# Kernel tuning notes

Hardware: AMD Instinct MI355X
Metric: run time of the kernel (lower is better)

The kernel has to match this reference:

```python
import jax, jax.numpy as jnp
import numpy as np

EPS = 1e-5


def setup_inputs() -> dict:
    key = jax.random.key(0)
    ks = jax.random.split(key, 6)
    b, n, x_len, h_len = 128, 512, 512, 512
    fan_in = x_len + h_len
    std = float(np.sqrt(2.0 / fan_in))  # kaiming_normal_ for [h_len, x_len+h_len]
    X = jax.random.normal(ks[0], (b, n, x_len), dtype=jnp.float32)
    W_a = jax.random.normal(ks[1], (h_len, fan_in), dtype=jnp.float32) * std
    W_g = jax.random.normal(ks[2], (h_len, fan_in), dtype=jnp.float32) * std
    b_a = jax.random.normal(ks[3], (h_len,), dtype=jnp.float32) * 0.02
    b_g = jax.random.normal(ks[4], (h_len,), dtype=jnp.float32) * 0.02
    gamma = jnp.ones((h_len,), dtype=jnp.float32)
    beta = jnp.zeros((h_len,), dtype=jnp.float32)
    return {"X": X, "W_a": W_a, "W_g": W_g, "b_a": b_a, "b_g": b_g,
            "gamma": gamma, "beta": beta}


def _layernorm(x, gamma, beta):
    mu = jnp.mean(x, axis=-1, keepdims=True)
    var = jnp.mean(jnp.square(x - mu), axis=-1, keepdims=True)
    return (x - mu) * jax.lax.rsqrt(var + EPS) * gamma + beta


def reference(X, W_a, W_g, b_a, b_g, gamma, beta):
    # X: [b, n, x_len]; recurrent scan over the time axis n.
    b, n, x_len = X.shape
    h_len = W_a.shape[0]

    def step(h, x_t):
        cat = jnp.concatenate([h, x_t], axis=-1)          # [b, h+x]
        alpha = jax.nn.sigmoid(cat @ W_g.T + b_g)          # [b, h]
        a = cat @ W_a.T + b_a                              # [b, h]
        h_tilde = alpha * jnp.tanh(a) + (1.0 - alpha) * a  # affine blend
        h_new = _layernorm(h_tilde, gamma, beta)           # dropout = identity (eval)
        return h_new, h_new

    h0 = jnp.zeros((b, h_len), dtype=X.dtype)
    _, ys = jax.lax.scan(step, h0, jnp.swapaxes(X, 0, 1))  # ys: [n, b, h]
    return jnp.swapaxes(ys, 0, 1)                          # [b, n, h]
```

## Files before the change

### kernel.cpp

```cpp
#include <hip/hip_runtime.h>
#include <math.h>

typedef _Float16 f16;
typedef _Float16 f16x8 __attribute__((ext_vector_type(8)));
typedef float f32x4 __attribute__((ext_vector_type(4)));
typedef unsigned long long u64;
typedef unsigned u32;

union U32H2 { unsigned u; f16 h[2]; };
union UV4H8 { uint4 u; f16x8 h; f16 e[8]; };

#define LN_EPS 1e-5f

__device__ __forceinline__ void st_u64g(u64* p, u64 v) {
    __hip_atomic_store(p, v, __ATOMIC_RELAXED, __HIP_MEMORY_SCOPE_AGENT);
}
__device__ __forceinline__ u64 ld_u64g(const u64* p) {
    return __hip_atomic_load(p, __ATOMIC_RELAXED, __HIP_MEMORY_SCOPE_AGENT);
}

__global__ __launch_bounds__(256) void init_ex(u64* p, int n) {
    const int i = blockIdx.x * 256 + threadIdx.x;
    if (i < n) p[i] = 0ull;
}

__global__ __launch_bounds__(256) void pack_wfrags(
    const float* __restrict__ Wa, const float* __restrict__ Wg,
    const float* __restrict__ gamma, uint4* __restrict__ WP)
{
    const int t = blockIdx.x * 256 + threadIdx.x;
    const int lane = t & 63;
    const int kf = (t >> 6) & 15;
    const int tile = t >> 10;
    const float* W = (tile < 32) ? Wa : Wg;
    const int col = (tile & 31) * 16 + (lane & 15);
    const int k0 = kf * 32 + (lane >> 4) * 8;
    const float* src = W + (size_t)col * 1024 + k0;
    UV4H8 u;
#pragma unroll
    for (int j = 0; j < 8; ++j) u.e[j] = (f16)(src[j] * gamma[k0 + j]);
    WP[t] = u.u;
}

__global__ __launch_bounds__(256) void pack_wx(
    const float* __restrict__ Wa, const float* __restrict__ Wg,
    uint4* __restrict__ WPx)
{
    const int t = blockIdx.x * 256 + threadIdx.x;
    const int lane = t & 63;
    const int kf = (t >> 6) & 15;
    const int tile = t >> 10;
    const float* W = (tile < 32) ? Wa : Wg;
    const int col = (tile & 31) * 16 + (lane & 15);
    const int k0 = kf * 32 + (lane >> 4) * 8;
    const float* src = W + (size_t)col * 1024 + 512 + k0;
    UV4H8 u;
#pragma unroll
    for (int j = 0; j < 8; ++j) u.e[j] = (f16)src[j];
    WPx[t] = u.u;
}

__global__ __launch_bounds__(64) void precompute_consts(
    const float* __restrict__ Wa, const float* __restrict__ Wg,
    const float* __restrict__ gamma, const float* __restrict__ beta,
    float* __restrict__ Cvec)
{
    const int o = blockIdx.x;
    const int l = threadIdx.x;
    const float* wa = Wa + (size_t)o * 1024;
    const float* wg = Wg + (size_t)o * 1024;
    float ca = 0.f, ga = 0.f, cg = 0.f, gg = 0.f;
    for (int k = l; k < 512; k += 64) {
        const float bk = beta[k], gk = gamma[k], a = wa[k], g = wg[k];
        ca += a * bk; ga += a * gk; cg += g * bk; gg += g * gk;
    }
#pragma unroll
    for (int m = 1; m < 64; m <<= 1) {
        ca += __shfl_xor(ca, m); ga += __shfl_xor(ga, m);
        cg += __shfl_xor(cg, m); gg += __shfl_xor(gg, m);
    }
    if (l == 0) {
        Cvec[o] = ca; Cvec[512 + o] = ga; Cvec[1024 + o] = cg; Cvec[1536 + o] = gg;
    }
}

__global__ __launch_bounds__(512) void pgemm16(
    const float* __restrict__ X, const uint4* __restrict__ WPx,
    const float* __restrict__ ba, const float* __restrict__ bg,
    float* __restrict__ Pa, f16* __restrict__ Pgh)
{
    __shared__ f16 As[128 * 64];
    const int tid = threadIdx.x;
    const int wv = tid >> 6, lane = tid & 63;
    const int bid = blockIdx.x;
    const int bn = bid & 7;
    const int bm = bid >> 3;
    const int m0 = bm * 128;
    const int tile = bn * 8 + wv;

    f16x8 Bf[16];
#pragma unroll
    for (int kf = 0; kf < 16; ++kf) {
        UV4H8 uu; uu.u = WPx[(size_t)(tile * 16 + kf) * 64 + lane];
        Bf[kf] = uu.h;
    }
    const int tcol = lane & 15;
    const float bias = (tile < 32) ? ba[tile * 16 + tcol]
                                   : bg[(tile - 32) * 16 + tcol];

    f32x4 acc[8];
#pragma unroll
    for (int mt = 0; mt < 8; ++mt) acc[mt] = (f32x4){0.f, 0.f, 0.f, 0.f};

    const int r = tid >> 2;
    const int c16 = (tid & 3) * 16;
    const int swzw = (r & 7) << 4;
    char* wbase = (char*)As + r * 128;
    const int arow = lane & 15;
    const int swzr = (arow & 7) << 4;
    const int hi = (lane >> 4) * 16;

    for (int kc = 0; kc < 8; ++kc) {
        {
            const float* src = X + (size_t)(m0 + r) * 512 + kc * 64 + c16;
            const float4 v0 = *(const float4*)(src);
            const float4 v1 = *(const float4*)(src + 4);
            const float4 v2 = *(const float4*)(src + 8);
            const float4 v3 = *(const float4*)(src + 12);
            UV4H8 o0, o1;
            o0.e[0] = (f16)v0.x; o0.e[1] = (f16)v0.y; o0.e[2] = (f16)v0.z; o0.e[3] = (f16)v0.w;
            o0.e[4] = (f16)v1.x; o0.e[5] = (f16)v1.y; o0.e[6] = (f16)v1.z; o0.e[7] = (f16)v1.w;
            o1.e[0] = (f16)v2.x; o1.e[1] = (f16)v2.y; o1.e[2] = (f16)v2.z; o1.e[3] = (f16)v2.w;
            o1.e[4] = (f16)v3.x; o1.e[5] = (f16)v3.y; o1.e[6] = (f16)v3.z; o1.e[7] = (f16)v3.w;
            *(uint4*)(wbase + ((c16 * 2) ^ swzw)) = o0.u;
            *(uint4*)(wbase + ((c16 * 2 + 16) ^ swzw)) = o1.u;
        }
        __syncthreads();
#pragma unroll
        for (int mt = 0; mt < 8; ++mt) {
            const char* rbase = (const char*)As + (mt * 16 + arow) * 128;
            const f16x8 Af0 = *(const f16x8*)(rbase + ((hi) ^ swzr));
            acc[mt] = __builtin_amdgcn_mfma_f32_16x16x32_f16(Af0, Bf[kc * 2], acc[mt], 0, 0, 0);
            const f16x8 Af1 = *(const f16x8*)(rbase + ((64 + hi) ^ swzr));
            acc[mt] = __builtin_amdgcn_mfma_f32_16x16x32_f16(Af1, Bf[kc * 2 + 1], acc[mt], 0, 0, 0);
        }
        __syncthreads();
    }

    const int drow = (lane >> 4) * 4;
    if (tile < 32) {
        const int col = tile * 16 + tcol;
#pragma unroll
        for (int mt = 0; mt < 8; ++mt)
#pragma unroll
            for (int i = 0; i < 4; ++i)
                Pa[(size_t)(m0 + mt * 16 + drow + i) * 512 + col] = acc[mt][i] + bias;
    } else {
        const int col = (tile - 32) * 16 + tcol;
#pragma unroll
        for (int mt = 0; mt < 8; ++mt)
#pragma unroll
            for (int i = 0; i < 4; ++i)
                Pgh[(size_t)(m0 + mt * 16 + drow + i) * 512 + col] = (f16)(acc[mt][i] + bias);
    }
}

__global__ __launch_bounds__(512, 1) void scan11(
    const uint4* __restrict__ WP, const float* __restrict__ gamma,
    const float* __restrict__ beta, const float* __restrict__ Cvec,
    float* po, const f16* __restrict__ Pgh,
    u64* __restrict__ THex)
{
    __shared__ f16 hn[16][512];
    __shared__ float Dx[16][132];

    const int tid = threadIdx.x;
    const int wv = tid >> 6, lane = tid & 63;
    const int bid = blockIdx.x;
    const int rg = bid >> 3, cb = bid & 7;
    const int c0 = cb * 64, r0 = rg * 16;

    const int tile = (wv < 4) ? (cb * 4 + wv) : (32 + cb * 4 + (wv - 4));
    f16x8 Bf[16];
#pragma unroll
    for (int kf = 0; kf < 16; ++kf) {
        UV4H8 uu; uu.u = WP[(size_t)(tile * 16 + kf) * 64 + lane];
        Bf[kf] = uu.h;
    }

    for (int i = tid; i < 16 * 256; i += 512) ((unsigned*)hn)[i] = 0u;

    const int rb = tid >> 5, u = tid & 31;
    const int col0 = c0 + 2 * u;
    const float Ca0 = Cvec[col0],        Ca1 = Cvec[col0 + 1];
    const float Ga0 = Cvec[512 + col0],  Ga1 = Cvec[512 + col0 + 1];
    const float Cg0 = Cvec[1024 + col0], Cg1 = Cvec[1024 + col0 + 1];
    const float Gg0 = Cvec[1536 + col0], Gg1 = Cvec[1536 + col0 + 1];
    const float gm0 = gamma[col0], gm1 = gamma[col0 + 1];
    const float bt0 = beta[col0],  bt1 = beta[col0 + 1];

    const int arow = lane & 15;
    const int hi16 = (lane >> 4) * 16;
    const int swzr = (arow & 7) << 4;
    const int swzw = (rb & 7) << 4;
    const char* hrow_r = (const char*)&hn[arow][0];
    char* hrow_w = (char*)&hn[rb][0];
    const int dr = (lane >> 4) * 4;
    const int dc = wv * 16 + (lane & 15);
    const size_t row = (size_t)(r0 + rb);

    u64* pub0 = THex + ((size_t)0 * 8 + rg) * 4096 + (size_t)rb * 256 + cb * 32 + u;
    u64* pub1 = THex + ((size_t)1 * 8 + rg) * 4096 + (size_t)rb * 256 + cb * 32 + u;
    const u64* pol0 = THex + ((size_t)0 * 8 + rg) * 4096 + (size_t)rb * 256 + u;
    const u64* pol1 = THex + ((size_t)1 * 8 + rg) * 4096 + (size_t)rb * 256 + u;

    float ht0, ht1;
    {
        const size_t orow = (row * 512 + 0) * 512 + col0;
        const float2 pa = *(const float2*)(po + orow);
        U32H2 pg; pg.u = *(const unsigned*)(Pgh + orow);
        const float a0 = pa.x, a1 = pa.y;
        const float g0 = (float)pg.h[0], g1 = (float)pg.h[1];
        const float al0 = 1.f / (1.f + __expf(-g0));
        const float al1 = 1.f / (1.f + __expf(-g1));
        const float ac0 = fminf(fmaxf(a0, -15.f), 15.f);
        const float ac1 = fminf(fmaxf(a1, -15.f), 15.f);
        const float e0 = __expf(2.f * ac0), e1 = __expf(2.f * ac1);
        const float th0 = (e0 - 1.f) / (e0 + 1.f);
        const float th1 = (e1 - 1.f) / (e1 + 1.f);
        ht0 = al0 * (th0 - a0) + a0;
        ht1 = al1 * (th1 - a1) + a1;
        U32H2 hw; hw.h[0] = (f16)ht0; hw.h[1] = (f16)ht1;
        st_u64g(pub0, ((u64)1u << 32) | (u64)hw.u);
    }

    for (int t = 1; t < 512; ++t) {
        const unsigned tg = (unsigned)t;
        const u64* hp = ((t - 1) & 1) ? pol1 : pol0;
        const size_t orow = (row * 512 + (size_t)t) * 512 + col0;
        const float2 pa = *(const float2*)(po + orow);
        U32H2 pg; pg.u = *(const unsigned*)(Pgh + orow);

        u64 v[8];
        for (;;) {
#pragma unroll
            for (int i = 0; i < 8; ++i) v[i] = ld_u64g(hp + i * 32);
            bool ok = true;
#pragma unroll
            for (int i = 0; i < 8; ++i) ok &= ((unsigned)(v[i] >> 32) == tg);
            if (ok) break;
        }

        float s1 = 0.f, s2 = 0.f;
#pragma unroll
        for (int i = 0; i < 8; ++i) {
            U32H2 hh; hh.u = (unsigned)v[i];
            const float x0 = (float)hh.h[0], x1 = (float)hh.h[1];
            s1 += x0 + x1; s2 += x0 * x0 + x1 * x1;
            *(u32*)(hrow_w + ((128 * i + 4 * u) ^ swzw)) = (unsigned)v[i];
        }
        __syncthreads();

#pragma unroll
        for (int m = 1; m < 32; m <<= 1) { s1 += __shfl_xor(s1, m); s2 += __shfl_xor(s2, m); }
        const float mu = s1 * (1.f / 512.f);
        const float var = s2 * (1.f / 512.f) - mu * mu;
        const float rs = rsqrtf(fmaxf(var, 0.f) + LN_EPS);
        const float murs = mu * rs;

        f32x4 acc0 = {0.f, 0.f, 0.f, 0.f};
        f32x4 acc1 = {0.f, 0.f, 0.f, 0.f};
#pragma unroll
        for (int kf = 0; kf < 8; ++kf) {
            const f16x8 Af0 = *(const f16x8*)(hrow_r + ((kf * 64 + hi16) ^ swzr));
            acc0 = __builtin_amdgcn_mfma_f32_16x16x32_f16(Af0, Bf[kf], acc0, 0, 0, 0);
            const f16x8 Af1 = *(const f16x8*)(hrow_r + (((kf + 8) * 64 + hi16) ^ swzr));
            acc1 = __builtin_amdgcn_mfma_f32_16x16x32_f16(Af1, Bf[kf + 8], acc1, 0, 0, 0);
        }
        Dx[dr + 0][dc] = acc0[0] + acc1[0];
        Dx[dr + 1][dc] = acc0[1] + acc1[1];
        Dx[dr + 2][dc] = acc0[2] + acc1[2];
        Dx[dr + 3][dc] = acc0[3] + acc1[3];
        __syncthreads();

        const float a0 = rs * Dx[rb][2 * u]          - murs * Ga0 + Ca0 + pa.x;
        const float a1 = rs * Dx[rb][2 * u + 1]      - murs * Ga1 + Ca1 + pa.y;
        const float g0 = rs * Dx[rb][64 + 2 * u]     - murs * Gg0 + Cg0 + (float)pg.h[0];
        const float g1 = rs * Dx[rb][64 + 2 * u + 1] - murs * Gg1 + Cg1 + (float)pg.h[1];
        const float al0 = 1.f / (1.f + __expf(-g0));
        const float al1 = 1.f / (1.f + __expf(-g1));
        const float ac0 = fminf(fmaxf(a0, -15.f), 15.f);
        const float ac1 = fminf(fmaxf(a1, -15.f), 15.f);
        const float e0 = __expf(2.f * ac0), e1 = __expf(2.f * ac1);
        const float th0 = (e0 - 1.f) / (e0 + 1.f);
        const float th1 = (e1 - 1.f) / (e1 + 1.f);
        const float nt0 = al0 * (th0 - a0) + a0;
        const float nt1 = al1 * (th1 - a1) + a1;

        {
            U32H2 hw; hw.h[0] = (f16)nt0; hw.h[1] = (f16)nt1;
            st_u64g((t & 1) ? pub1 : pub0,
                    ((u64)(unsigned)(t + 1) << 32) | (u64)hw.u);
            po[orow - 512]     = (ht0 - mu) * rs * gm0 + bt0;
            po[orow - 512 + 1] = (ht1 - mu) * rs * gm1 + bt1;
            ht0 = nt0; ht1 = nt1;
        }
        __syncthreads();
    }

    {
        u64 v[8];
        for (;;) {
#pragma unroll
            for (int i = 0; i < 8; ++i) v[i] = ld_u64g(pol1 + i * 32);
            bool ok = true;
#pragma unroll
            for (int i = 0; i < 8; ++i) ok &= ((unsigned)(v[i] >> 32) == 512u);
            if (ok) break;
        }
        float s1 = 0.f, s2 = 0.f;
#pragma unroll
        for (int i = 0; i < 8; ++i) {
            U32H2 hh; hh.u = (unsigned)v[i];
            const float x0 = (float)hh.h[0], x1 = (float)hh.h[1];
            s1 += x0 + x1; s2 += x0 * x0 + x1 * x1;
        }
#pragma unroll
        for (int m = 1; m < 32; m <<= 1) { s1 += __shfl_xor(s1, m); s2 += __shfl_xor(s2, m); }
        const float mu = s1 * (1.f / 512.f);
        const float var = s2 * (1.f / 512.f) - mu * mu;
        const float rs = rsqrtf(fmaxf(var, 0.f) + LN_EPS);
        const size_t orow = (row * 512 + 511) * 512 + col0;
        po[orow]     = (ht0 - mu) * rs * gm0 + bt0;
        po[orow + 1] = (ht1 - mu) * rs * gm1 + bt1;
    }
}

extern "C" void kernel_launch(void* const* d_in, const int* in_sizes, int n_in,
                              void* d_out, int out_size, void* d_ws, size_t ws_size,
                              hipStream_t stream) {
    (void)in_sizes; (void)n_in; (void)out_size; (void)ws_size;
    const float* X     = (const float*)d_in[0];
    const float* Wa    = (const float*)d_in[1];
    const float* Wg    = (const float*)d_in[2];
    const float* ba    = (const float*)d_in[3];
    const float* bg    = (const float*)d_in[4];
    const float* gamma = (const float*)d_in[5];
    const float* beta  = (const float*)d_in[6];
    float* out = (float*)d_out;

    char* ws = (char*)d_ws;
    f16*    Pgh  = (f16*)ws;
    uint4*  WP   = (uint4*)(ws + 67108864);
    u64*    THex = (u64*)(ws + 68157440);
    float*  Cvec = (float*)(ws + 68681728);
    uint4*  WPx  = (uint4*)(ws + 68689920);

    init_ex<<<dim3(256), dim3(256), 0, stream>>>(THex, 65536);
    pack_wfrags<<<dim3(256), dim3(256), 0, stream>>>(Wa, Wg, gamma, WP);
    pack_wx<<<dim3(256), dim3(256), 0, stream>>>(Wa, Wg, WPx);
    precompute_consts<<<dim3(512), dim3(64), 0, stream>>>(Wa, Wg, gamma, beta, Cvec);
    pgemm16<<<dim3(4096), dim3(512), 0, stream>>>(X, WPx, ba, bg, out, Pgh);

    void* args[] = { (void*)&WP, (void*)&gamma, (void*)&beta, (void*)&Cvec,
                     (void*)&out, (void*)&Pgh, (void*)&THex };
    hipLaunchCooperativeKernel((const void*)scan11, dim3(64), dim3(512),
                               args, 0, stream);
}
```

Baseline: 1.500 ms.

## Compute gate epilogue directly in MFMA waves and publish 32-bit per-column flags

Restructures the recurrent scan step so four waves each compute both the a and g MFMA tiles and run the sigmoid/tanh blend straight from accumulators. This removes the Dx shared-memory round trip and one of the two block barriers per timestep. Each column's f16 state is published as a 32-bit tagged word instead of a packed 64-bit pair. LayerNorm statistics are shared through small shared arrays, and the normalized output is rebuilt from the exchanged h values. The cost is that half the waves sit idle during the matmul and epilogue, and the consumer must check two tags per 64-bit load.

```diff
diff --git a/kernel.cpp b/kernel.cpp
--- a/kernel.cpp
+++ b/kernel.cpp
@@ -9,10 +9,11 @@
 
 union U32H2 { unsigned u; f16 h[2]; };
 union UV4H8 { uint4 u; f16x8 h; f16 e[8]; };
+union H1 { unsigned short s; f16 h; };
 
 #define LN_EPS 1e-5f
 
-__device__ __forceinline__ void st_u64g(u64* p, u64 v) {
+__device__ __forceinline__ void st_u32g(u32* p, u32 v) {
     __hip_atomic_store(p, v, __ATOMIC_RELAXED, __HIP_MEMORY_SCOPE_AGENT);
 }
 __device__ __forceinline__ u64 ld_u64g(const u64* p) {
@@ -165,81 +166,84 @@
     }
 }
 
-__global__ __launch_bounds__(512, 1) void scan11(
+__global__ __launch_bounds__(512, 1) void scan12(
     const uint4* __restrict__ WP, const float* __restrict__ gamma,
     const float* __restrict__ beta, const float* __restrict__ Cvec,
     float* po, const f16* __restrict__ Pgh,
-    u64* __restrict__ THex)
+    u32* __restrict__ THex)
 {
     __shared__ f16 hn[16][512];
-    __shared__ float Dx[16][132];
+    __shared__ float mu_s[16], rs_s[16];
 
     const int tid = threadIdx.x;
     const int wv = tid >> 6, lane = tid & 63;
     const int bid = blockIdx.x;
     const int rg = bid >> 3, cb = bid & 7;
     const int c0 = cb * 64, r0 = rg * 16;
-
-    const int tile = (wv < 4) ? (cb * 4 + wv) : (32 + cb * 4 + (wv - 4));
-    f16x8 Bf[16];
-#pragma unroll
-    for (int kf = 0; kf < 16; ++kf) {
-        UV4H8 uu; uu.u = WP[(size_t)(tile * 16 + kf) * 64 + lane];
-        Bf[kf] = uu.h;
-    }
-
-    for (int i = tid; i < 16 * 256; i += 512) ((unsigned*)hn)[i] = 0u;
+    const bool mfmaw = (wv < 4);
+
+    const int wsel = wv & 3;
+    f16x8 Bfa[16], Bfg[16];
+    {
+        const int ta = cb * 4 + wsel, tg_ = 32 + cb * 4 + wsel;
+#pragma unroll
+        for (int kf = 0; kf < 16; ++kf) {
+            UV4H8 ua; ua.u = WP[(size_t)(ta * 16 + kf) * 64 + lane];
+            Bfa[kf] = ua.h;
+            UV4H8 ug; ug.u = WP[(size_t)(tg_ * 16 + kf) * 64 + lane];
+            Bfg[kf] = ug.h;
+        }
+    }
+    const int mcol = c0 + wsel * 16 + (lane & 15);
+    const int dr = (lane >> 4) * 4;
+    const float CaM = Cvec[mcol],        GaM = Cvec[512 + mcol];
+    const float CgM = Cvec[1024 + mcol], GgM = Cvec[1536 + mcol];
 
     const int rb = tid >> 5, u = tid & 31;
     const int col0 = c0 + 2 * u;
-    const float Ca0 = Cvec[col0],        Ca1 = Cvec[col0 + 1];
-    const float Ga0 = Cvec[512 + col0],  Ga1 = Cvec[512 + col0 + 1];
-    const float Cg0 = Cvec[1024 + col0], Cg1 = Cvec[1024 + col0 + 1];
-    const float Gg0 = Cvec[1536 + col0], Gg1 = Cvec[1536 + col0 + 1];
     const float gm0 = gamma[col0], gm1 = gamma[col0 + 1];
     const float bt0 = beta[col0],  bt1 = beta[col0 + 1];
-
     const int arow = lane & 15;
     const int hi16 = (lane >> 4) * 16;
     const int swzr = (arow & 7) << 4;
     const int swzw = (rb & 7) << 4;
     const char* hrow_r = (const char*)&hn[arow][0];
     char* hrow_w = (char*)&hn[rb][0];
-    const int dr = (lane >> 4) * 4;
-    const int dc = wv * 16 + (lane & 15);
-    const size_t row = (size_t)(r0 + rb);
-
-    u64* pub0 = THex + ((size_t)0 * 8 + rg) * 4096 + (size_t)rb * 256 + cb * 32 + u;
-    u64* pub1 = THex + ((size_t)1 * 8 + rg) * 4096 + (size_t)rb * 256 + cb * 32 + u;
-    const u64* pol0 = THex + ((size_t)0 * 8 + rg) * 4096 + (size_t)rb * 256 + u;
-    const u64* pol1 = THex + ((size_t)1 * 8 + rg) * 4096 + (size_t)rb * 256 + u;
-
-    float ht0, ht1;
-    {
-        const size_t orow = (row * 512 + 0) * 512 + col0;
-        const float2 pa = *(const float2*)(po + orow);
-        U32H2 pg; pg.u = *(const unsigned*)(Pgh + orow);
-        const float a0 = pa.x, a1 = pa.y;
-        const float g0 = (float)pg.h[0], g1 = (float)pg.h[1];
-        const float al0 = 1.f / (1.f + __expf(-g0));
-        const float al1 = 1.f / (1.f + __expf(-g1));
-        const float ac0 = fminf(fmaxf(a0, -15.f), 15.f);
-        const float ac1 = fminf(fmaxf(a1, -15.f), 15.f);
-        const float e0 = __expf(2.f * ac0), e1 = __expf(2.f * ac1);
-        const float th0 = (e0 - 1.f) / (e0 + 1.f);
-        const float th1 = (e1 - 1.f) / (e1 + 1.f);
-        ht0 = al0 * (th0 - a0) + a0;
-        ht1 = al1 * (th1 - a1) + a1;
-        U32H2 hw; hw.h[0] = (f16)ht0; hw.h[1] = (f16)ht1;
-        st_u64g(pub0, ((u64)1u << 32) | (u64)hw.u);
+    const size_t prow = (size_t)(r0 + rb);
+
+    const u64* pol0 = (const u64*)(THex + ((size_t)(0 * 8 + rg) * 16 + rb) * 512) + u;
+    const u64* pol1 = (const u64*)(THex + ((size_t)(1 * 8 + rg) * 16 + rb) * 512) + u;
+
+    if (mfmaw) {
+#pragma unroll
+        for (int i = 0; i < 4; ++i) {
+            const size_t idx = ((size_t)(r0 + dr + i) * 512 + 0) * 512 + mcol;
+            const float a0 = po[idx];
+            const float g0 = (float)Pgh[idx];
+            const float al = 1.f / (1.f + __expf(-g0));
+            const float ac = fminf(fmaxf(a0, -15.f), 15.f);
+            const float e = __expf(2.f * ac);
+            const float th = (e - 1.f) / (e + 1.f);
+            const float ht = al * (th - a0) + a0;
+            H1 hb; hb.h = (f16)ht;
+            st_u32g(THex + ((size_t)(0 * 8 + rg) * 16 + dr + i) * 512 + mcol,
+                    (1u << 16) | (u32)hb.s);
+        }
     }
 
     for (int t = 1; t < 512; ++t) {
         const unsigned tg = (unsigned)t;
         const u64* hp = ((t - 1) & 1) ? pol1 : pol0;
-        const size_t orow = (row * 512 + (size_t)t) * 512 + col0;
-        const float2 pa = *(const float2*)(po + orow);
-        U32H2 pg; pg.u = *(const unsigned*)(Pgh + orow);
+
+        float paM[4]; unsigned short pgM[4];
+        if (mfmaw) {
+#pragma unroll
+            for (int i = 0; i < 4; ++i) {
+                const size_t idx = ((size_t)(r0 + dr + i) * 512 + (size_t)t) * 512 + mcol;
+                paM[i] = po[idx];
+                pgM[i] = *(const unsigned short*)(Pgh + idx);
+            }
+        }
 
         u64 v[8];
         for (;;) {
@@ -247,65 +251,68 @@
             for (int i = 0; i < 8; ++i) v[i] = ld_u64g(hp + i * 32);
             bool ok = true;
 #pragma unroll
-            for (int i = 0; i < 8; ++i) ok &= ((unsigned)(v[i] >> 32) == tg);
+            for (int i = 0; i < 8; ++i)
+                ok &= (((unsigned)(v[i] >> 16) & 0xFFFFu) == tg) &
+                      ((unsigned)(v[i] >> 48) == tg);
             if (ok) break;
         }
 
         float s1 = 0.f, s2 = 0.f;
 #pragma unroll
         for (int i = 0; i < 8; ++i) {
-            U32H2 hh; hh.u = (unsigned)v[i];
-            const float x0 = (float)hh.h[0], x1 = (float)hh.h[1];
+            H1 a, b; a.s = (unsigned short)v[i]; b.s = (unsigned short)(v[i] >> 32);
+            const float x0 = (float)a.h, x1 = (float)b.h;
             s1 += x0 + x1; s2 += x0 * x0 + x1 * x1;
-            *(u32*)(hrow_w + ((128 * i + 4 * u) ^ swzw)) = (unsigned)v[i];
-        }
-        __syncthreads();
-
+            const u32 w32 = (u32)(v[i] & 0xFFFFu) | ((u32)(v[i] >> 32) << 16);
+            *(u32*)(hrow_w + ((128 * i + 4 * u) ^ swzw)) = w32;
+        }
 #pragma unroll
         for (int m = 1; m < 32; m <<= 1) { s1 += __shfl_xor(s1, m); s2 += __shfl_xor(s2, m); }
         const float mu = s1 * (1.f / 512.f);
         const float var = s2 * (1.f / 512.f) - mu * mu;
         const float rs = rsqrtf(fmaxf(var, 0.f) + LN_EPS);
-        const float murs = mu * rs;
-
-        f32x4 acc0 = {0.f, 0.f, 0.f, 0.f};
-        f32x4 acc1 = {0.f, 0.f, 0.f, 0.f};
-#pragma unroll
-        for (int kf = 0; kf < 8; ++kf) {
-            const f16x8 Af0 = *(const f16x8*)(hrow_r + ((kf * 64 + hi16) ^ swzr));
-            acc0 = __builtin_amdgcn_mfma_f32_16x16x32_f16(Af0, Bf[kf], acc0, 0, 0, 0);
-            const f16x8 Af1 = *(const f16x8*)(hrow_r + (((kf + 8) * 64 + hi16) ^ swzr));
-            acc1 = __builtin_amdgcn_mfma_f32_16x16x32_f16(Af1, Bf[kf + 8], acc1, 0, 0, 0);
-        }
-        Dx[dr + 0][dc] = acc0[0] + acc1[0];
-        Dx[dr + 1][dc] = acc0[1] + acc1[1];
-        Dx[dr + 2][dc] = acc0[2] + acc1[2];
-        Dx[dr + 3][dc] = acc0[3] + acc1[3];
+        if (u == 0) { mu_s[rb] = mu; rs_s[rb] = rs; }
+
+        {
+            H1 a, b; a.s = (unsigned short)v[cb]; b.s = (unsigned short)(v[cb] >> 32);
+            const size_t o = (prow * 512 + (size_t)(t - 1)) * 512 + col0;
+            po[o]     = ((float)a.h - mu) * rs * gm0 + bt0;
+            po[o + 1] = ((float)b.h - mu) * rs * gm1 + bt1;
+        }
         __syncthreads();
 
-        const float a0 = rs * Dx[rb][2 * u]          - murs * Ga0 + Ca0 + pa.x;
-        const float a1 = rs * Dx[rb][2 * u + 1]      - murs * Ga1 + Ca1 + pa.y;
-        const float g0 = rs * Dx[rb][64 + 2 * u]     - murs * Gg0 + Cg0 + (float)pg.h[0];
-        const float g1 = rs * Dx[rb][64 + 2 * u + 1] - murs * Gg1 + Cg1 + (float)pg.h[1];
-        const float al0 = 1.f / (1.f + __expf(-g0));
-        const float al1 = 1.f / (1.f + __expf(-g1));
-        const float ac0 = fminf(fmaxf(a0, -15.f), 15.f);
-        const float ac1 = fminf(fmaxf(a1, -15.f), 15.f);
-        const float e0 = __expf(2.f * ac0), e1 = __expf(2.f * ac1);
-        const float th0 = (e0 - 1.f) / (e0 + 1.f);
-        const float th1 = (e1 - 1.f) / (e1 + 1.f);
-        const float nt0 = al0 * (th0 - a0) + a0;
-        const float nt1 = al1 * (th1 - a1) + a1;
-
-        {
-            U32H2 hw; hw.h[0] = (f16)nt0; hw.h[1] = (f16)nt1;
-            st_u64g((t & 1) ? pub1 : pub0,
-                    ((u64)(unsigned)(t + 1) << 32) | (u64)hw.u);
-            po[orow - 512]     = (ht0 - mu) * rs * gm0 + bt0;
-            po[orow - 512 + 1] = (ht1 - mu) * rs * gm1 + bt1;
-            ht0 = nt0; ht1 = nt1;
-        }
-        __syncthreads();
+        if (mfmaw) {
+            f32x4 acc0 = {0.f, 0.f, 0.f, 0.f};
+            f32x4 acc1 = {0.f, 0.f, 0.f, 0.f};
+            f32x4 acc2 = {0.f, 0.f, 0.f, 0.f};
+            f32x4 acc3 = {0.f, 0.f, 0.f, 0.f};
+#pragma unroll
+            for (int kf = 0; kf < 8; ++kf) {
+                const f16x8 Af0 = *(const f16x8*)(hrow_r + ((kf * 64 + hi16) ^ swzr));
+                acc0 = __builtin_amdgcn_mfma_f32_16x16x32_f16(Af0, Bfa[kf], acc0, 0, 0, 0);
+                acc2 = __builtin_amdgcn_mfma_f32_16x16x32_f16(Af0, Bfg[kf], acc2, 0, 0, 0);
+                const f16x8 Af1 = *(const f16x8*)(hrow_r + (((kf + 8) * 64 + hi16) ^ swzr));
+                acc1 = __builtin_amdgcn_mfma_f32_16x16x32_f16(Af1, Bfa[kf + 8], acc1, 0, 0, 0);
+                acc3 = __builtin_amdgcn_mfma_f32_16x16x32_f16(Af1, Bfg[kf + 8], acc3, 0, 0, 0);
+            }
+            const u32 ptag = (u32)(t + 1) << 16;
+            u32* pb = THex + ((size_t)((t & 1) * 8 + rg) * 16 + dr) * 512 + mcol;
+#pragma unroll
+            for (int i = 0; i < 4; ++i) {
+                const float mui = mu_s[dr + i], rsi = rs_s[dr + i];
+                const float mursi = mui * rsi;
+                const float a0 = rsi * (acc0[i] + acc1[i]) - mursi * GaM + CaM + paM[i];
+                H1 pgh; pgh.s = pgM[i];
+                const float g0 = rsi * (acc2[i] + acc3[i]) - mursi * GgM + CgM + (float)pgh.h;
+                const float al = 1.f / (1.f + __expf(-g0));
+                const float ac = fminf(fmaxf(a0, -15.f), 15.f);
+                const float e = __expf(2.f * ac);
+                const float th = (e - 1.f) / (e + 1.f);
+                const float nt = al * (th - a0) + a0;
+                H1 hb; hb.h = (f16)nt;
+                st_u32g(pb + (size_t)i * 512, ptag | (u32)hb.s);
+            }
+        }
     }
 
     {
@@ -315,14 +322,16 @@
             for (int i = 0; i < 8; ++i) v[i] = ld_u64g(pol1 + i * 32);
             bool ok = true;
 #pragma unroll
-            for (int i = 0; i < 8; ++i) ok &= ((unsigned)(v[i] >> 32) == 512u);
+            for (int i = 0; i < 8; ++i)
+                ok &= (((unsigned)(v[i] >> 16) & 0xFFFFu) == 512u) &
+                      ((unsigned)(v[i] >> 48) == 512u);
             if (ok) break;
         }
         float s1 = 0.f, s2 = 0.f;
 #pragma unroll
         for (int i = 0; i < 8; ++i) {
-            U32H2 hh; hh.u = (unsigned)v[i];
-            const float x0 = (float)hh.h[0], x1 = (float)hh.h[1];
+            H1 a, b; a.s = (unsigned short)v[i]; b.s = (unsigned short)(v[i] >> 32);
+            const float x0 = (float)a.h, x1 = (float)b.h;
             s1 += x0 + x1; s2 += x0 * x0 + x1 * x1;
         }
 #pragma unroll
@@ -330,9 +339,10 @@
         const float mu = s1 * (1.f / 512.f);
         const float var = s2 * (1.f / 512.f) - mu * mu;
         const float rs = rsqrtf(fmaxf(var, 0.f) + LN_EPS);
-        const size_t orow = (row * 512 + 511) * 512 + col0;
-        po[orow]     = (ht0 - mu) * rs * gm0 + bt0;
-        po[orow + 1] = (ht1 - mu) * rs * gm1 + bt1;
+        H1 a, b; a.s = (unsigned short)v[cb]; b.s = (unsigned short)(v[cb] >> 32);
+        const size_t o = (prow * 512 + 511) * 512 + col0;
+        po[o]     = ((float)a.h - mu) * rs * gm0 + bt0;
+        po[o + 1] = ((float)b.h - mu) * rs * gm1 + bt1;
     }
 }
 
@@ -352,11 +362,11 @@
     char* ws = (char*)d_ws;
     f16*    Pgh  = (f16*)ws;
     uint4*  WP   = (uint4*)(ws + 67108864);
-    u64*    THex = (u64*)(ws + 68157440);
+    u32*    THex = (u32*)(ws + 68157440);
     float*  Cvec = (float*)(ws + 68681728);
     uint4*  WPx  = (uint4*)(ws + 68689920);
 
-    init_ex<<<dim3(256), dim3(256), 0, stream>>>(THex, 65536);
+    init_ex<<<dim3(256), dim3(256), 0, stream>>>((u64*)THex, 65536);
     pack_wfrags<<<dim3(256), dim3(256), 0, stream>>>(Wa, Wg, gamma, WP);
     pack_wx<<<dim3(256), dim3(256), 0, stream>>>(Wa, Wg, WPx);
     precompute_consts<<<dim3(512), dim3(64), 0, stream>>>(Wa, Wg, gamma, beta, Cvec);
@@ -364,6 +374,6 @@
 
     void* args[] = { (void*)&WP, (void*)&gamma, (void*)&beta, (void*)&Cvec,
                      (void*)&out, (void*)&Pgh, (void*)&THex };
-    hipLaunchCooperativeKernel((const void*)scan11, dim3(64), dim3(512),
+    hipLaunchCooperativeKernel((const void*)scan12, dim3(64), dim3(512),
                                args, 0, stream);
 }
```

After: 1.891 ms. +26.1%, slower.
